# Kernel optimization log

Measured on AMD Instinct MI355X. Metric: run time of the kernel, lower is better.

The kernel has to match this reference:

```python
import jax, jax.numpy as jnp
import numpy as np

B, T, C, D = 4, 2048, 48, 512
L = 16                    # transcript length per video (distinct labels)
K = 9                     # bdy_kernel
CS = 15                   # cs_kernel
N_TR = L - 1
N_CAND = 3 * N_TR         # candidate_mul * pt_num
WIN_LEN = int(T / L * 0.15)   # int(t / t_len * win_scale)
ALPHA, BETA, GAMMA, TEMP = 1.0, 1.0, 0.1, 0.1
LOG2 = float(np.log(2.0))

def _bdy_kernel():
    ker = np.zeros((K, K), np.float32)
    c = K // 2
    ker[:c, :c] = 1; ker[c:, c:] = 1
    ker[:c, c:] = -1; ker[c:, :c] = -1
    ker[c, c] = 0
    return jnp.asarray(ker)

BDY_KER = _bdy_kernel()

def bdy_score_fn(prob):
    # prob: [T, C]; sliding windows of size K over time (zero padded)
    c = K // 2
    pad = jnp.pad(prob, ((c, c), (0, 0)))
    win = pad[jnp.arange(T)[:, None] + jnp.arange(K)[None, :]]       # [T,K,C]
    p = win[:, :, None, :]                                           # [T,K,1,C]
    m = (p + win[:, None, :, :]) / 2                                 # [T,K,K,C]
    # torch F.kl_div((m+1e-32).log(), p) = p*(log p - log(m+1e-32)), xlogy(0)=0
    kl = jnp.sum(jnp.where(p > 0, p * (jnp.log(jnp.where(p > 0, p, 1.0)) - jnp.log(m + 1e-32)), 0.0), -1)
    js = (kl + jnp.swapaxes(kl, 1, 2)) / 2
    js = -(js / LOG2 * 2 - 1)                                        # [T,K,K]
    return jnp.mean(BDY_KER[None] * js, axis=(-1, -2))               # [T]

def dp(cls_score):
    # cls_score: [N_TR, N_CAND]; min-cost alignment DP, inner jj-loop vectorized
    cost = -cls_score
    n_tr, n_x = N_TR, N_CAND
    W = 2 * n_tr + 1
    col = jnp.arange(W)
    inf = jnp.float32(jnp.inf)
    tr_at = jnp.clip(col // 2, 0, n_tr - 1)
    even = (col % 2 == 0)
    ge2 = col >= 2

    def init_cols(ii):
        c0 = jnp.where(ii < n_x - n_tr, 0.0, inf)
        c1 = jnp.where(ii <= n_x - n_tr, cost[0, ii], inf)
        d1 = jnp.where(ii <= n_x - n_tr, 1, 0).astype(jnp.int32)
        return c0, c1, d1

    c0, c1, d1 = init_cols(0)
    row0 = jnp.full((W,), inf).at[0].set(c0).at[1].set(c1)
    dir0 = jnp.zeros((W,), jnp.int32).at[1].set(d1)

    def step(prev, ii):
        dm1 = jnp.concatenate([jnp.full((1,), inf), prev[:-1]])
        dm2 = jnp.concatenate([jnp.full((2,), inf), prev[:-2]])
        c_at = cost[:, ii][tr_at]
        even_val = jnp.minimum(prev, dm1)
        even_dir = jnp.where(prev < dm1, 0, 1).astype(jnp.int32)
        odd_val = c_at + jnp.minimum(dm1, dm2)
        odd_dir = jnp.where(dm1 < dm2, 1, 2).astype(jnp.int32)
        c0, c1, d1 = init_cols(ii)
        new = jnp.where(ge2, jnp.where(even, even_val, odd_val), inf)
        new = new.at[0].set(c0).at[1].set(c1)
        dirs = jnp.where(ge2, jnp.where(even, even_dir, odd_dir), 0).astype(jnp.int32)
        dirs = dirs.at[1].set(d1)
        return new, dirs

    last, dirs = jax.lax.scan(step, row0, jnp.arange(1, n_x))
    dir_mat = jnp.concatenate([dir0[None], dirs], 0)                 # [n_x, W]
    cur_j0 = jnp.where(last[2 * n_tr] < last[2 * n_tr - 1], 2 * n_tr, 2 * n_tr - 1).astype(jnp.int32)

    def bt(cur_j, x):
        ii, dir_row = x
        is_odd = (cur_j % 2) == 1
        out_idx = jnp.where(is_odd, cur_j // 2, jnp.int32(n_tr))     # n_tr = OOB -> dropped
        new_j = cur_j - dir_row[cur_j]
        return new_j, (out_idx, ii.astype(jnp.int32))

    _, (oi, ovals) = jax.lax.scan(bt, cur_j0, (jnp.arange(n_x), dir_mat), reverse=True)
    return jnp.zeros((n_tr,), jnp.int32).at[oi].set(ovals, mode='drop')

def detect(logit, tr):
    # logit: [T,C] (detached), tr: [L] ints -> boundary frame indices [N_TR]
    prob = jax.nn.softmax(logit, -1)
    score = bdy_score_fn(prob).at[0].set(-jnp.inf)
    backup = score
    pos = jnp.arange(T)

    def pick(s, _):
        i = jnp.argmax(s)
        return jnp.where(jnp.abs(pos - i) <= WIN_LEN, -jnp.inf, s), i

    _, cand = jax.lax.scan(pick, score, None, length=N_CAND)
    cand = jnp.sort(cand)                                            # [N_CAND]
    # class-transition score at candidate points
    cc = CS // 2
    pairs = jnp.pad(prob[:, tr], ((cc, cc), (0, 0)))                 # [T+2cc, L]
    win = pairs[cand[:, None] + jnp.arange(CS)[None, :]]             # [N_CAND, CS, L]
    first, second = win[:, :, :-1], win[:, :, 1:]
    k0 = jnp.where(jnp.arange(CS) < cc, 1.0, -1.0)[None, :, None]
    cls = jnp.sum(k0 * (first - second), axis=1) / (2 * CS)          # [N_CAND, N_TR]
    cls = cls.T + backup[cand][None, :]                              # [N_TR, N_CAND]
    return cand[dp(cls)]

def _forward(tok_logit, fr_logit, vid_multi_hot, feat, mask, transcript):
    y = vid_multi_hot
    tok_loss = jnp.mean(-(y * jax.nn.log_sigmoid(tok_logit) + (1 - y) * jax.nn.log_sigmoid(-tok_logit)))
    # boundary detection on detached logits
    bdy = jax.vmap(detect)(jax.lax.stop_gradient(fr_logit), transcript)   # [B, N_TR]
    pse = jax.vmap(lambda b, tr: tr[jnp.sum(jnp.arange(T)[:, None] >= b[None, :], axis=1)])(bdy, transcript)
    # frame CE (bgw==1.0 path, full mask so no -100 labels)
    logp = jax.nn.log_softmax(fr_logit, -1)
    ce = -jnp.take_along_axis(logp, pse[..., None], axis=-1)[..., 0]
    m = mask.astype(ce.dtype)
    fr_loss = jnp.sum(ce * m) / jnp.sum(m)
    # global-local contrast
    tok_feat = jax.lax.stop_gradient(feat[:, :C, :])
    fr_feat = feat[:, C:, :]

    def glc_one(tok, fr, pse_i, tr, m_i):
        labels = jnp.sort(tr)                                        # = unique(pse[mask]), distinct labels
        oh = (pse_i[None, :] == labels[:, None]).astype(fr.dtype) * m_i[None, :]
        cnt = jnp.maximum(jnp.sum(oh, 1, keepdims=True), 1.0)
        la = (oh @ fr) / cnt
        la = la / jnp.maximum(jnp.linalg.norm(la, axis=-1, keepdims=True), 1e-12)
        tk = tok / jnp.maximum(jnp.linalg.norm(tok, axis=-1, keepdims=True), 1e-12)
        sim = (la @ tk.T) / TEMP                                     # [L, C]
        return jnp.mean(-jnp.take_along_axis(jax.nn.log_softmax(sim, -1), labels[:, None], axis=-1))

    glc_loss = jnp.mean(jax.vmap(glc_one)(tok_feat, fr_feat, pse, transcript, mask.astype(feat.dtype)))
    return ALPHA * tok_loss + BETA * fr_loss + GAMMA * glc_loss

def setup_inputs() -> dict:
    key = jax.random.key(0)
    ks = jax.random.split(key, 5)
    tok_logit = jax.random.normal(ks[0], (B, C), jnp.float32)
    fr_logit = jax.random.normal(ks[1], (B, T, C), jnp.float32)
    mask = jnp.ones((B, T), bool)
    transcript = jax.vmap(lambda k: jax.random.permutation(k, C)[:L])(jax.random.split(ks[2], B)).astype(jnp.int32)
    vid_multi_hot = jax.random.uniform(ks[3], (B, C), jnp.float32)
    feat = jax.random.normal(ks[4], (B, C + T, D), jnp.float32)
    return {"epoch": 5, "tok_logit": tok_logit, "fr_logit": fr_logit, "mask": mask,
            "transcript": transcript, "vid_multi_hot": vid_multi_hot, "feat": feat}

def reference(epoch, tok_logit, fr_logit, mask, transcript, vid_multi_hot, feat):
    # epoch >= warm_epc (=0), so the full loss path runs
    return _forward(tok_logit, fr_logit, vid_multi_hot, feat, mask, transcript)
```

## Files before the change

### kernel.cpp

```cpp
#include <hip/hip_runtime.h>
#include <math.h>

#define BB 4
#define TT 2048
#define CC 48
#define DD 512
#define LL 16
#define NTR 15
#define NCAND 45
#define WINLEN 19
#define CSW 15
#define CCHALF 7

static __device__ __forceinline__ float wave_reduce_sum(float v) {
    for (int off = 32; off; off >>= 1) v += __shfl_down(v, off);
    return v;
}

#define DPPMAX(x, ctrl) fmaxf((x), __int_as_float(__builtin_amdgcn_update_dpp( \
    __float_as_int(x), __float_as_int(x), (ctrl), 0xF, 0xF, false)))

__global__ __launch_bounds__(256) void k_lse(const float* __restrict__ fr,
                                             float* __restrict__ lse) {
    int row = blockIdx.x * 4 + (threadIdx.x >> 6);
    int lane = threadIdx.x & 63;
    float xv = (lane < CC) ? fr[(size_t)row * CC + lane] : -INFINITY;
    float m = xv;
    for (int off = 32; off; off >>= 1) m = fmaxf(m, __shfl_down(m, off));
    m = __shfl(m, 0);
    float e = (lane < CC) ? __expf(xv - m) : 0.f;
    float s = wave_reduce_sum(e);
    if (lane == 0) lse[row] = m + __logf(s);
}

__global__ __launch_bounds__(64) void k_score(const float* __restrict__ fr,
                                              const float* __restrict__ lse,
                                              float* __restrict__ score) {
    int row = blockIdx.x;
    int b = row / TT, t = row % TT;
    __shared__ float sp[9][CC];
    __shared__ float slp[9][CC];
    __shared__ float lse_s[9];
    int tid = threadIdx.x;
    if (tid < 9) {
        int r = t - 4 + tid;
        lse_s[tid] = (r >= 0 && r < TT) ? lse[b * TT + r] : 0.f;
    }
    __syncthreads();
    for (int idx = tid; idx < 9 * CC; idx += 64) {
        int i = idx / CC, c = idx - (idx / CC) * CC;
        int r = t - 4 + i;
        float pv = 0.f, lv = 0.f;
        if (r >= 0 && r < TT) {
            float x = fr[((size_t)b * TT + r) * CC + c];
            lv = x - lse_s[i];
            pv = __expf(lv);
        }
        sp[i][c] = pv;
        slp[i][c] = lv;
    }
    __syncthreads();
    float acc = 0.f;
    for (int idx = tid; idx < 4 * CC; idx += 64) {
        int i = idx / CC, c = idx - (idx / CC) * CC;
        acc += -2.f * sp[i][c] * slp[i][c];
    }
    for (int item = tid; item < 36 * CC; item += 64) {
        int pidx = item / CC, c = item - pidx * CC;
        int i = 0, rem = pidx;
        while (rem >= 8 - i) { rem -= 8 - i; ++i; }
        int j = i + 1 + rem;
        float wgt = ((i < 4) == (j < 4)) ? 1.f : -1.f;
        float pi = sp[i][c], pj = sp[j][c];
        float logm = __logf(0.5f * (pi + pj) + 1e-32f);
        acc -= wgt * (pi + pj) * logm;
    }
    acc = wave_reduce_sum(acc);
    if (tid == 0) {
        const float SC = -2.0f / (81.0f * 0.6931471805599453f);
        score[row] = (t == 0) ? -INFINITY : SC * acc;
    }
}

__global__ __launch_bounds__(256) void k_pickdp(const float* __restrict__ fr,
                                                const float* __restrict__ lse,
                                                const float* __restrict__ score,
                                                const int* __restrict__ transcript,
                                                int* __restrict__ labels_out,
                                                int* __restrict__ seg_start,
                                                int* __restrict__ seg_end,
                                                float* __restrict__ fr_part) {
    int b = blockIdx.x;
    __shared__ int cl[NCAND];
    __shared__ float cost[NTR][NCAND];
    __shared__ int tr_s[LL];
    __shared__ int cand_s[NCAND];
    __shared__ float backup_s[NCAND];
    __shared__ signed char dir_mat[NCAND][32];
    __shared__ int bdy_s[NTR];
    __shared__ int rank_s[LL];
    __shared__ float rv[2][4];
    __shared__ int rp[2][4];
    __shared__ float redf[4];
    int tid = threadIdx.x;
    int wave = tid >> 6, lane = tid & 63;
    if (tid < LL) tr_s[tid] = transcript[b * LL + tid];

    float v[8];
    {
        const float4* sp4 = (const float4*)(score + (size_t)b * TT);
        float4 va = sp4[2 * tid], vb = sp4[2 * tid + 1];
        v[0] = va.x; v[1] = va.y; v[2] = va.z; v[3] = va.w;
        v[4] = vb.x; v[5] = vb.y; v[6] = vb.z; v[7] = vb.w;
    }
    for (int it = 0; it < NCAND; ++it) {
        float best = -INFINITY; int bi = 0;
        #pragma unroll
        for (int k = 7; k >= 0; --k)
            if (v[k] >= best) { best = v[k]; bi = k; }
        int pos = tid * 8 + bi;
        float m = best;
        m = DPPMAX(m, 0x111); m = DPPMAX(m, 0x112);
        m = DPPMAX(m, 0x114); m = DPPMAX(m, 0x118);
        m = DPPMAX(m, 0x142); m = DPPMAX(m, 0x143);
        float wmax = __int_as_float(__builtin_amdgcn_readlane(__float_as_int(m), 63));
        unsigned long long ball = __ballot(best == wmax);
        int sl = (int)(__ffsll((long long)ball) - 1);
        int wpos = __builtin_amdgcn_readlane(pos, sl);
        if (lane == 0) { rv[it & 1][wave] = wmax; rp[it & 1][wave] = wpos; }
        __syncthreads();
        float bvv = -INFINITY; int mp = 0x7fffffff;
        #pragma unroll
        for (int w = 0; w < 4; ++w) {
            float vv = rv[it & 1][w]; int pp = rp[it & 1][w];
            if (vv > bvv || (vv == bvv && pp < mp)) { bvv = vv; mp = pp; }
        }
        if (tid == 0) cl[it] = mp;
        int lo = mp - WINLEN, hi = mp + WINLEN;
        #pragma unroll
        for (int k = 0; k < 8; ++k) {
            int t = tid * 8 + k;
            if (t >= lo && t <= hi) v[k] = -INFINITY;
        }
    }
    __syncthreads();
    if (tid < NCAND) {
        int my = cl[tid];
        int rank = 0;
        for (int i = 0; i < NCAND; ++i) rank += (cl[i] < my) ? 1 : 0;
        cand_s[rank] = my;
    }
    __syncthreads();
    if (tid < NCAND) backup_s[tid] = score[(size_t)b * TT + cand_s[tid]];
    __syncthreads();

    for (int e = tid; e < NTR * NCAND; e += 256) {
        int j = e / NCAND, ii = e - (e / NCAND) * NCAND;
        int cpos = cand_s[ii];
        int trj = tr_s[j], trj1 = tr_s[j + 1];
        float sum = 0.f;
        for (int k = 0; k < CSW; ++k) {
            int r = cpos - CCHALF + k;
            float a = 0.f, d2 = 0.f;
            if (r >= 0 && r < TT) {
                size_t ro = (size_t)b * TT + r;
                float ls = lse[ro];
                a  = __expf(fr[ro * CC + trj]  - ls);
                d2 = __expf(fr[ro * CC + trj1] - ls);
            }
            sum += ((k < CCHALF) ? 1.f : -1.f) * (a - d2);
        }
        cost[j][ii] = -(sum / 30.f + backup_s[ii]);
    }
    __syncthreads();

    if (tid < 64) {
        float prev = INFINITY;
        if (tid == 0) prev = 0.f;
        if (tid == 1) prev = cost[0][0];
        if (tid < 31) dir_mat[0][tid] = (tid == 1) ? (signed char)1 : (signed char)0;
        for (int ii = 1; ii < NCAND; ++ii) {
            float dm1 = __shfl_up(prev, 1); if (tid < 1) dm1 = INFINITY;
            float dm2 = __shfl_up(prev, 2); if (tid < 2) dm2 = INFINITY;
            int trat = tid >> 1; if (trat > NTR - 1) trat = NTR - 1;
            float c_at = cost[trat][ii];
            float ev = fminf(prev, dm1);
            int ed = (prev < dm1) ? 0 : 1;
            float ov = c_at + fminf(dm1, dm2);
            int od = (dm1 < dm2) ? 1 : 2;
            float nv; int nd;
            if (tid >= 2) {
                if ((tid & 1) == 0) { nv = ev; nd = ed; }
                else { nv = ov; nd = od; }
            } else { nv = INFINITY; nd = 0; }
            if (tid == 0) { nv = (ii < NCAND - NTR) ? 0.f : INFINITY; nd = 0; }
            if (tid == 1) {
                nv = (ii <= NCAND - NTR) ? cost[0][ii] : INFINITY;
                nd = (ii <= NCAND - NTR) ? 1 : 0;
            }
            prev = nv;
            if (tid < 31) dir_mat[ii][tid] = (signed char)nd;
        }
        float v29 = __shfl(prev, 29);
        float v30 = __shfl(prev, 30);
        if (tid == 0) {
            int cur = (v30 < v29) ? 30 : 29;
            for (int ii = NCAND - 1; ii >= 0; --ii) {
                if (cur & 1) bdy_s[cur >> 1] = cand_s[ii];
                cur -= (int)dir_mat[ii][cur];
            }
            int lab[LL];
            for (int i2 = 0; i2 < LL; ++i2) lab[i2] = tr_s[i2];
            for (int a2 = 1; a2 < LL; ++a2) {
                int key = lab[a2]; int b2 = a2 - 1;
                while (b2 >= 0 && lab[b2] > key) { lab[b2 + 1] = lab[b2]; --b2; }
                lab[b2 + 1] = key;
            }
            for (int i2 = 0; i2 < LL; ++i2) labels_out[b * LL + i2] = lab[i2];
            for (int j2 = 0; j2 < LL; ++j2) {
                int r2 = 0;
                for (int l2 = 0; l2 < LL; ++l2) if (lab[l2] == tr_s[j2]) r2 = l2;
                rank_s[j2] = r2;
            }
            for (int j2 = 0; j2 < LL; ++j2) {
                int st = (j2 == 0) ? 0 : bdy_s[j2 - 1];
                int en = (j2 == LL - 1) ? TT : bdy_s[j2];
                seg_start[b * LL + rank_s[j2]] = st;
                seg_end[b * LL + rank_s[j2]] = en;
            }
        }
    }
    __syncthreads();

    float facc = 0.f;
    for (int t = tid; t < TT; t += 256) {
        int cnt = 0;
        for (int j = 0; j < NTR; ++j) cnt += (t >= bdy_s[j]) ? 1 : 0;
        int pv = tr_s[cnt];
        size_t ro = (size_t)b * TT + t;
        facc += lse[ro] - fr[ro * CC + pv];
    }
    facc = wave_reduce_sum(facc);
    if (lane == 0) redf[wave] = facc;
    __syncthreads();
    if (tid == 0) fr_part[b] = redf[0] + redf[1] + redf[2] + redf[3];
}

__global__ __launch_bounds__(256) void k_laglc(const float* __restrict__ feat,
                                               const int* __restrict__ seg_start,
                                               const int* __restrict__ seg_end,
                                               const int* __restrict__ labels,
                                               float* __restrict__ terms) {
    int l = blockIdx.x, b = blockIdx.y;
    int st = seg_start[b * LL + l], en = seg_end[b * LL + l];
    int tid = threadIdx.x;
    int wave = tid >> 6, lane = tid & 63;
    const float* frf = feat + ((size_t)b * (CC + TT) + CC) * DD;
    __shared__ float part[4][DD];
    __shared__ float la_s[DD];
    __shared__ float sim_s[CC];
    __shared__ float red[4];
    __shared__ float s_inv_nla;
    float4 a0 = {0,0,0,0}, a1 = {0,0,0,0};
    for (int r = st + wave; r < en; r += 4) {
        const float4* p = (const float4*)(frf + (size_t)r * DD);
        float4 v0 = p[lane];
        float4 v1 = p[64 + lane];
        a0.x += v0.x; a0.y += v0.y; a0.z += v0.z; a0.w += v0.w;
        a1.x += v1.x; a1.y += v1.y; a1.z += v1.z; a1.w += v1.w;
    }
    ((float4*)part[wave])[lane] = a0;
    ((float4*)part[wave])[64 + lane] = a1;
    __syncthreads();
    float ssl = 0.f;
    for (int idx = tid; idx < DD; idx += 256) {
        float s = part[0][idx] + part[1][idx] + part[2][idx] + part[3][idx];
        la_s[idx] = s;
        ssl += s * s;
    }
    ssl = wave_reduce_sum(ssl);
    if (lane == 0) red[wave] = ssl;
    __syncthreads();
    if (tid == 0)
        s_inv_nla = 10.0f / fmaxf(sqrtf(red[0] + red[1] + red[2] + red[3]), 1e-12f);
    __syncthreads();
    for (int c = wave; c < CC; c += 4) {
        const float4* tr = (const float4*)(feat + ((size_t)b * (CC + TT) + c) * DD);
        const float4* ls = (const float4*)la_s;
        float dot = 0.f, vv = 0.f;
        for (int j = lane; j < DD / 4; j += 64) {
            float4 a = ls[j]; float4 w = tr[j];
            dot += a.x * w.x + a.y * w.y + a.z * w.z + a.w * w.w;
            vv  += w.x * w.x + w.y * w.y + w.z * w.z + w.w * w.w;
        }
        dot = wave_reduce_sum(dot);
        vv  = wave_reduce_sum(vv);
        if (lane == 0)
            sim_s[c] = dot * s_inv_nla / fmaxf(sqrtf(vv), 1e-12f);
    }
    __syncthreads();
    if (tid == 0) {
        float mx = -INFINITY;
        for (int c = 0; c < CC; ++c) mx = fmaxf(mx, sim_s[c]);
        float se = 0.f;
        for (int c = 0; c < CC; ++c) se += expf(sim_s[c] - mx);
        int lab = labels[b * LL + l];
        terms[b * LL + l] = (mx + logf(se)) - sim_s[lab];
    }
}

__global__ __launch_bounds__(256) void k_combine(const float* __restrict__ tok_logit,
                                                 const float* __restrict__ vid,
                                                 const float* __restrict__ fr_part,
                                                 const float* __restrict__ terms,
                                                 float* __restrict__ out) {
    int tid = threadIdx.x;
    __shared__ float red[4];
    float acc = 0.f;
    if (tid < BB * CC) {
        float x = tok_logit[tid], y = vid[tid];
        float lsp = fminf(x, 0.f) - log1pf(expf(-fabsf(x)));
        float lsn = fminf(-x, 0.f) - log1pf(expf(-fabsf(x)));
        acc = -(y * lsp + (1.f - y) * lsn);
    }
    float w = wave_reduce_sum(acc);
    if ((tid & 63) == 0) red[tid >> 6] = w;
    __syncthreads();
    if (tid == 0) {
        float s_tok = (red[0] + red[1] + red[2] + red[3]) / (float)(BB * CC);
        float sfr = fr_part[0] + fr_part[1] + fr_part[2] + fr_part[3];
        float s_fr = sfr / (float)(BB * TT);
        float g = 0.f;
        for (int i = 0; i < BB * LL; ++i) g += terms[i];
        float glc = g / (float)(BB * LL);
        out[0] = s_tok + s_fr + 0.1f * glc;
    }
}

extern "C" void kernel_launch(void* const* d_in, const int* in_sizes, int n_in,
                              void* d_out, int out_size, void* d_ws, size_t ws_size,
                              hipStream_t stream) {
    (void)in_sizes; (void)n_in; (void)out_size; (void)ws_size;
    const float* tok_logit  = (const float*)d_in[1];
    const float* fr_logit   = (const float*)d_in[2];
    const int*   transcript = (const int*)d_in[4];
    const float* vid        = (const float*)d_in[5];
    const float* feat       = (const float*)d_in[6];

    char* ws = (char*)d_ws;
    float* lse     = (float*)(ws + 0);
    float* score   = (float*)(ws + 32768);
    float* terms   = (float*)(ws + 65536);
    float* fr_part = (float*)(ws + 65792);
    int*   labels  = (int*)(ws + 66048);
    int*   seg_st  = (int*)(ws + 66304);
    int*   seg_en  = (int*)(ws + 66560);
    float* out     = (float*)d_out;

    k_lse<<<BB * TT / 4, 256, 0, stream>>>(fr_logit, lse);
    k_score<<<BB * TT, 64, 0, stream>>>(fr_logit, lse, score);
    k_pickdp<<<BB, 256, 0, stream>>>(fr_logit, lse, score, transcript,
                                     labels, seg_st, seg_en, fr_part);
    k_laglc<<<dim3(LL, BB), 256, 0, stream>>>(feat, seg_st, seg_en, labels, terms);
    k_combine<<<1, 256, 0, stream>>>(tok_logit, vid, fr_part, terms, out);
}
```

Baseline: 199.4 us.

## Split segment-mean GLC into row-parallel atomic accumulation, dot, and term kernels

```diff
diff --git a/kernel.cpp b/kernel.cpp
--- a/kernel.cpp
+++ b/kernel.cpp
@@ -87,9 +87,9 @@
                                                 const float* __restrict__ score,
                                                 const int* __restrict__ transcript,
                                                 int* __restrict__ labels_out,
-                                                int* __restrict__ seg_start,
-                                                int* __restrict__ seg_end,
-                                                float* __restrict__ fr_part) {
+                                                int* __restrict__ rowmap,
+                                                float* __restrict__ fr_part,
+                                                float* __restrict__ la) {
     int b = blockIdx.x;
     __shared__ int cl[NCAND];
     __shared__ float cost[NTR][NCAND];
@@ -106,6 +106,13 @@
     int wave = tid >> 6, lane = tid & 63;
     if (tid < LL) tr_s[tid] = transcript[b * LL + tid];
 
+    {
+        float4 z = {0.f, 0.f, 0.f, 0.f};
+        float4* lz = (float4*)(la + (size_t)b * LL * DD);
+        #pragma unroll
+        for (int i = 0; i < LL * DD / 4 / 256; ++i) lz[i * 256 + tid] = z;
+    }
+
     float v[8];
     {
         const float4* sp4 = (const float4*)(score + (size_t)b * TT);
@@ -159,6 +166,7 @@
         int cpos = cand_s[ii];
         int trj = tr_s[j], trj1 = tr_s[j + 1];
         float sum = 0.f;
+        #pragma unroll
         for (int k = 0; k < CSW; ++k) {
             int r = cpos - CCHALF + k;
             float a = 0.f, d2 = 0.f;
@@ -209,34 +217,27 @@
                 if (cur & 1) bdy_s[cur >> 1] = cand_s[ii];
                 cur -= (int)dir_mat[ii][cur];
             }
-            int lab[LL];
-            for (int i2 = 0; i2 < LL; ++i2) lab[i2] = tr_s[i2];
-            for (int a2 = 1; a2 < LL; ++a2) {
-                int key = lab[a2]; int b2 = a2 - 1;
-                while (b2 >= 0 && lab[b2] > key) { lab[b2 + 1] = lab[b2]; --b2; }
-                lab[b2 + 1] = key;
-            }
-            for (int i2 = 0; i2 < LL; ++i2) labels_out[b * LL + i2] = lab[i2];
-            for (int j2 = 0; j2 < LL; ++j2) {
-                int r2 = 0;
-                for (int l2 = 0; l2 < LL; ++l2) if (lab[l2] == tr_s[j2]) r2 = l2;
-                rank_s[j2] = r2;
-            }
-            for (int j2 = 0; j2 < LL; ++j2) {
-                int st = (j2 == 0) ? 0 : bdy_s[j2 - 1];
-                int en = (j2 == LL - 1) ? TT : bdy_s[j2];
-                seg_start[b * LL + rank_s[j2]] = st;
-                seg_end[b * LL + rank_s[j2]] = en;
-            }
-        }
+        }
+    }
+    __syncthreads();
+
+    if (tid < LL) {
+        int myv = tr_s[tid];
+        int r2 = 0;
+        #pragma unroll
+        for (int l2 = 0; l2 < LL; ++l2) r2 += (tr_s[l2] < myv) ? 1 : 0;
+        rank_s[tid] = r2;
+        labels_out[b * LL + r2] = myv;
     }
     __syncthreads();
 
     float facc = 0.f;
     for (int t = tid; t < TT; t += 256) {
         int cnt = 0;
+        #pragma unroll
         for (int j = 0; j < NTR; ++j) cnt += (t >= bdy_s[j]) ? 1 : 0;
         int pv = tr_s[cnt];
+        rowmap[b * TT + t] = rank_s[cnt];
         size_t ro = (size_t)b * TT + t;
         facc += lse[ro] - fr[ro * CC + pv];
     }
@@ -246,67 +247,96 @@
     if (tid == 0) fr_part[b] = redf[0] + redf[1] + redf[2] + redf[3];
 }
 
-__global__ __launch_bounds__(256) void k_laglc(const float* __restrict__ feat,
-                                               const int* __restrict__ seg_start,
-                                               const int* __restrict__ seg_end,
-                                               const int* __restrict__ labels,
-                                               float* __restrict__ terms) {
-    int l = blockIdx.x, b = blockIdx.y;
-    int st = seg_start[b * LL + l], en = seg_end[b * LL + l];
+__global__ __launch_bounds__(256) void k_la(const float* __restrict__ feat,
+                                            const int* __restrict__ rowmap,
+                                            float* __restrict__ la) {
+    int b = blockIdx.y;
+    int t0 = blockIdx.x * 32;
+    int tid = threadIdx.x;
+    const float* frf = feat + ((size_t)b * (CC + TT) + CC) * DD;
+    __shared__ int rm[32];
+    if (tid < 32) rm[tid] = rowmap[b * TT + t0 + tid];
+    __syncthreads();
+    float ax = 0.f, ay = 0.f;
+    int cur = rm[0];
+    for (int k = 0; k < 32; ++k) {
+        int r = rm[k];
+        if (r != cur) {
+            float* dst = la + ((size_t)b * LL + cur) * DD + tid * 2;
+            atomicAdd(dst, ax);
+            atomicAdd(dst + 1, ay);
+            ax = 0.f; ay = 0.f; cur = r;
+        }
+        const float2* p = (const float2*)(frf + (size_t)(t0 + k) * DD);
+        float2 v = p[tid];
+        ax += v.x; ay += v.y;
+    }
+    float* dst = la + ((size_t)b * LL + cur) * DD + tid * 2;
+    atomicAdd(dst, ax);
+    atomicAdd(dst + 1, ay);
+}
+
+__global__ __launch_bounds__(256) void k_glc(const float* __restrict__ feat,
+                                             const float* __restrict__ la,
+                                             float* __restrict__ dots,
+                                             float* __restrict__ ntk) {
+    int c = blockIdx.x, b = blockIdx.y;
+    __shared__ float tok_s[DD];
+    __shared__ float redv[4];
     int tid = threadIdx.x;
     int wave = tid >> 6, lane = tid & 63;
-    const float* frf = feat + ((size_t)b * (CC + TT) + CC) * DD;
-    __shared__ float part[4][DD];
-    __shared__ float la_s[DD];
-    __shared__ float sim_s[CC];
-    __shared__ float red[4];
-    __shared__ float s_inv_nla;
-    float4 a0 = {0,0,0,0}, a1 = {0,0,0,0};
-    for (int r = st + wave; r < en; r += 4) {
-        const float4* p = (const float4*)(frf + (size_t)r * DD);
-        float4 v0 = p[lane];
-        float4 v1 = p[64 + lane];
-        a0.x += v0.x; a0.y += v0.y; a0.z += v0.z; a0.w += v0.w;
-        a1.x += v1.x; a1.y += v1.y; a1.z += v1.z; a1.w += v1.w;
-    }
-    ((float4*)part[wave])[lane] = a0;
-    ((float4*)part[wave])[64 + lane] = a1;
-    __syncthreads();
-    float ssl = 0.f;
-    for (int idx = tid; idx < DD; idx += 256) {
-        float s = part[0][idx] + part[1][idx] + part[2][idx] + part[3][idx];
-        la_s[idx] = s;
-        ssl += s * s;
-    }
-    ssl = wave_reduce_sum(ssl);
-    if (lane == 0) red[wave] = ssl;
+    const float* tr = feat + ((size_t)b * (CC + TT) + c) * DD;
+    float2 tv = ((const float2*)tr)[tid];
+    ((float2*)tok_s)[tid] = tv;
+    float vv = tv.x * tv.x + tv.y * tv.y;
+    vv = wave_reduce_sum(vv);
+    if (lane == 0) redv[wave] = vv;
     __syncthreads();
     if (tid == 0)
-        s_inv_nla = 10.0f / fmaxf(sqrtf(red[0] + red[1] + red[2] + red[3]), 1e-12f);
-    __syncthreads();
-    for (int c = wave; c < CC; c += 4) {
-        const float4* tr = (const float4*)(feat + ((size_t)b * (CC + TT) + c) * DD);
-        const float4* ls = (const float4*)la_s;
-        float dot = 0.f, vv = 0.f;
-        for (int j = lane; j < DD / 4; j += 64) {
-            float4 a = ls[j]; float4 w = tr[j];
+        ntk[b * CC + c] = fmaxf(sqrtf(redv[0] + redv[1] + redv[2] + redv[3]), 1e-12f);
+    for (int l = wave; l < LL; l += 4) {
+        const float4* lar = (const float4*)(la + ((size_t)b * LL + l) * DD);
+        const float4* ts = (const float4*)tok_s;
+        float dot = 0.f;
+        #pragma unroll
+        for (int jj = 0; jj < 2; ++jj) {
+            int j = lane + jj * 64;
+            float4 a = lar[j]; float4 w = ts[j];
             dot += a.x * w.x + a.y * w.y + a.z * w.z + a.w * w.w;
-            vv  += w.x * w.x + w.y * w.y + w.z * w.z + w.w * w.w;
         }
         dot = wave_reduce_sum(dot);
-        vv  = wave_reduce_sum(vv);
-        if (lane == 0)
-            sim_s[c] = dot * s_inv_nla / fmaxf(sqrtf(vv), 1e-12f);
-    }
-    __syncthreads();
-    if (tid == 0) {
-        float mx = -INFINITY;
-        for (int c = 0; c < CC; ++c) mx = fmaxf(mx, sim_s[c]);
-        float se = 0.f;
-        for (int c = 0; c < CC; ++c) se += expf(sim_s[c] - mx);
-        int lab = labels[b * LL + l];
-        terms[b * LL + l] = (mx + logf(se)) - sim_s[lab];
-    }
+        if (lane == 0) dots[((size_t)b * LL + l) * CC + c] = dot;
+    }
+}
+
+__global__ __launch_bounds__(64) void k_term(const float* __restrict__ la,
+                                             const float* __restrict__ dots,
+                                             const float* __restrict__ ntk,
+                                             const int* __restrict__ labels,
+                                             float* __restrict__ terms) {
+    int l = blockIdx.x, b = blockIdx.y;
+    int lane = threadIdx.x;
+    const float4* lar = (const float4*)(la + ((size_t)b * LL + l) * DD);
+    float ss = 0.f;
+    #pragma unroll
+    for (int jj = 0; jj < 2; ++jj) {
+        float4 a = lar[lane + jj * 64];
+        ss += a.x * a.x + a.y * a.y + a.z * a.z + a.w * a.w;
+    }
+    ss = wave_reduce_sum(ss);
+    float nla = fmaxf(sqrtf(__shfl(ss, 0)), 1e-12f);
+    float sim = -INFINITY;
+    if (lane < CC)
+        sim = dots[((size_t)b * LL + l) * CC + lane] * 10.0f / (nla * ntk[b * CC + lane]);
+    float mx = sim;
+    for (int off = 32; off; off >>= 1) mx = fmaxf(mx, __shfl_down(mx, off));
+    mx = __shfl(mx, 0);
+    float e = (lane < CC) ? expf(sim - mx) : 0.f;
+    float se = wave_reduce_sum(e);
+    se = __shfl(se, 0);
+    int lab = labels[b * LL + l];
+    float sim_lab = __shfl(sim, lab);
+    if (lane == 0) terms[b * LL + l] = (mx + logf(se)) - sim_lab;
 }
 
 __global__ __launch_bounds__(256) void k_combine(const float* __restrict__ tok_logit,
@@ -316,6 +346,7 @@
                                                  float* __restrict__ out) {
     int tid = threadIdx.x;
     __shared__ float red[4];
+    __shared__ float gterm;
     float acc = 0.f;
     if (tid < BB * CC) {
         float x = tok_logit[tid], y = vid[tid];
@@ -325,14 +356,17 @@
     }
     float w = wave_reduce_sum(acc);
     if ((tid & 63) == 0) red[tid >> 6] = w;
+    if (tid < 64) {
+        float g = terms[tid];
+        g = wave_reduce_sum(g);
+        if (tid == 0) gterm = g;
+    }
     __syncthreads();
     if (tid == 0) {
         float s_tok = (red[0] + red[1] + red[2] + red[3]) / (float)(BB * CC);
         float sfr = fr_part[0] + fr_part[1] + fr_part[2] + fr_part[3];
         float s_fr = sfr / (float)(BB * TT);
-        float g = 0.f;
-        for (int i = 0; i < BB * LL; ++i) g += terms[i];
-        float glc = g / (float)(BB * LL);
+        float glc = gterm / (float)(BB * LL);
         out[0] = s_tok + s_fr + 0.1f * glc;
     }
 }
@@ -350,17 +384,21 @@
     char* ws = (char*)d_ws;
     float* lse     = (float*)(ws + 0);
     float* score   = (float*)(ws + 32768);
-    float* terms   = (float*)(ws + 65536);
-    float* fr_part = (float*)(ws + 65792);
-    int*   labels  = (int*)(ws + 66048);
-    int*   seg_st  = (int*)(ws + 66304);
-    int*   seg_en  = (int*)(ws + 66560);
+    float* la      = (float*)(ws + 65536);
+    float* dots    = (float*)(ws + 196608);
+    float* ntk     = (float*)(ws + 208896);
+    float* terms   = (float*)(ws + 209664);
+    float* fr_part = (float*)(ws + 209920);
+    int*   labels  = (int*)(ws + 210176);
+    int*   rowmap  = (int*)(ws + 210432);
     float* out     = (float*)d_out;
 
     k_lse<<<BB * TT / 4, 256, 0, stream>>>(fr_logit, lse);
     k_score<<<BB * TT, 64, 0, stream>>>(fr_logit, lse, score);
     k_pickdp<<<BB, 256, 0, stream>>>(fr_logit, lse, score, transcript,
-                                     labels, seg_st, seg_en, fr_part);
-    k_laglc<<<dim3(LL, BB), 256, 0, stream>>>(feat, seg_st, seg_en, labels, terms);
+                                     labels, rowmap, fr_part, la);
+    k_la<<<dim3(TT / 32, BB), 256, 0, stream>>>(feat, rowmap, la);
+    k_glc<<<dim3(CC, BB), 256, 0, stream>>>(feat, la, dots, ntk);
+    k_term<<<dim3(LL, BB), 64, 0, stream>>>(la, dots, ntk, labels, terms);
     k_combine<<<1, 256, 0, stream>>>(tok_logit, vid, fr_part, terms, out);
 }
```

New measurement: 171.3 us. 14.1% less time.
